# Performance work log

Measured on AMD Instinct MI355X. Metric: run time of the kernel, lower is better.

Reference implementation:

```python
import math
import jax
import jax.numpy as jnp
import numpy as np

GRID = 12  # distance + 1 for distance-11 surface code


def _ln(x, s, b):
    m = jnp.mean(x, axis=-1, keepdims=True)
    v = jnp.mean((x - m) ** 2, axis=-1, keepdims=True)
    return (x - m) / jnp.sqrt(v + 1e-5) * s + b


def _gelu(x):
    return jax.nn.gelu(x, approximate=False)  # torch F.gelu default = exact erf


def _forward(meas, event, leak, event_leak, bias, pm_w, pm_b, pe_w, pe_b, pl_w, pl_b, pel_w, pel_b,
             stab_emb, cyc_emb, er_ln_s, er_ln_b, er_fc1_w, er_fc1_b, er_fc2_w, er_fc2_b,
             ln1_s, ln1_b, Wb, Wq, bq, Wk, bk, Wv, bv, Wo, bo, ln2_s, ln2_b,
             f1_w, f1_b, f2_w, f2_b, conv_w, conv_b, lnf_s, lnf_b,
             P, sc_w, sc_b, dr_w, dr_b, rb1_w, rb1_b, rb2_w, rb2_b, out_w, out_b,
             stab_ids, cycle_ids):
    B, T, S = meas.shape
    L, Hh, _, da = Wq.shape
    dm = Wv.shape[-1]
    d = P.shape[0]

    # per-head additive attention bias, identical across cycles: (L,B,H,S,S)
    Bp = jnp.einsum('bijd,ldh->lbhij', bias, Wb)
    scale = 1.0 / jnp.sqrt(jnp.asarray(da, meas.dtype))
    pos_emb = stab_emb[stab_ids]  # (S, d)

    def embed(t):
        h = (meas[:, t, :, None] * pm_w + pm_b
             + event[:, t, :, None] * pe_w + pe_b
             + leak[:, t, :, None] * pl_w + pl_b
             + event_leak[:, t, :, None] * pel_w + pel_b
             + pos_emb[None] + cyc_emb[cycle_ids[t]][None, None, :])
        for r in range(er_fc1_w.shape[0]):
            hn = _ln(h, er_ln_s[r], er_ln_b[r])
            h = h + jnp.matmul(_gelu(jnp.matmul(hn, er_fc1_w[r]) + er_fc1_b[r]), er_fc2_w[r]) + er_fc2_b[r]
        return h

    X = jnp.zeros((B, S, d), meas.dtype)
    for t in range(T):  # recurrent application of RNNCore over cycles
        X = (X + embed(t)) / jnp.sqrt(jnp.asarray(2.0, meas.dtype))
        for l in range(L):
            Xn = _ln(X, ln1_s[l], ln1_b[l])
            Q = jnp.einsum('bsd,hde->bhse', Xn, Wq[l]) + bq[l][None, :, None, :]
            Kt = jnp.einsum('bsd,hde->bhse', Xn, Wk[l]) + bk[l][None, :, None, :]
            V = jnp.einsum('bsd,hdm->bhsm', Xn, Wv[l]) + bv[l][None, :, None, :]
            Sc = jnp.einsum('bhqe,bhke->bhqk', Q, Kt) + Bp[l]  # bias added BEFORE 1/sqrt(da)
            A = jax.nn.softmax(Sc * scale, axis=-1)
            O = jnp.einsum('bhqk,bhkm->bhqm', A, V)
            Y = O.transpose(0, 2, 1, 3).reshape(B, S, Hh * dm)
            X = X + jnp.matmul(Y, Wo[l]) + bo[l]
            Xn = _ln(X, ln2_s[l], ln2_b[l])
            Yf = jnp.matmul(Xn, f1_w[l]) + f1_b[l]
            a, g = jnp.split(Yf, 2, axis=-1)
            X = X + jnp.matmul(_gelu(a) * g, f2_w[l]) + f2_b[l]
            # conv block: residual depth-mixing Conv1d(k=3, SAME) over the stabilizer axis
            xc = jnp.transpose(X, (0, 2, 1))  # (B, d, S)
            c = jax.lax.conv_general_dilated(xc, conv_w[l], (1,), 'SAME',
                                             dimension_numbers=('NCH', 'OIH', 'NCH'))
            X = X + _gelu(jnp.transpose(c + conv_b[l][None, :, None], (0, 2, 1)))

    # readout
    Xn = _ln(X, lnf_s, lnf_b)
    pad = jnp.broadcast_to(P, (B, GRID * GRID - S, d))  # empty grid cells filled with P
    grid = jnp.concatenate([Xn, pad], axis=1).reshape(B, GRID, GRID, d).transpose(0, 3, 1, 2)
    x = jax.lax.conv_general_dilated(grid, sc_w, (2, 2), 'VALID',
                                     dimension_numbers=('NCHW', 'OIHW', 'NCHW')) + sc_b[None, :, None, None]
    x = _gelu(x)
    x = jnp.einsum('bdhw,rd->brhw', x, dr_w) + dr_b[None, :, None, None]
    x = _gelu(x)
    x = x.mean(axis=2)  # basis 'z': pool over grid rows -> (B, rd, K)
    Kk = x.shape[2]
    x = x.transpose(0, 2, 1).reshape(B * Kk, -1)
    for r in range(rb1_w.shape[0]):
        x = x + jnp.matmul(_gelu(jnp.matmul(x, rb1_w[r]) + rb1_b[r]), rb2_w[r]) + rb2_b[r]
    logits = (jnp.matmul(x, out_w) + out_b).reshape(B, Kk).mean(axis=1)
    return logits


def setup_inputs() -> dict:
    key = jax.random.key(0)
    ks = iter(jax.random.split(key, 100))

    def rn(shape, s=0.02):
        return (s * jax.random.normal(next(ks), shape)).astype(jnp.float32)

    B, T, S, d = 16, 8, 120, 128
    L, H, da, dm, db = 2, 4, 32, 32, 32
    rd, nrb, ncyc = 48, 16, 32
    z = lambda *sh: jnp.zeros(sh, jnp.float32)
    o = lambda *sh: jnp.ones(sh, jnp.float32)
    inp = {
        'meas': jax.random.uniform(next(ks), (B, T, S), jnp.float32),
        'event': jax.random.uniform(next(ks), (B, T, S), jnp.float32),
        'leak': jax.random.uniform(next(ks), (B, T, S), jnp.float32),
        'event_leak': jax.random.uniform(next(ks), (B, T, S), jnp.float32),
        'bias': rn((B, S, S, db), 0.5),
        'pm_w': rn((d,)), 'pm_b': z(d),
        'pe_w': rn((d,)), 'pe_b': z(d),
        'pl_w': rn((d,)), 'pl_b': z(d),
        'pel_w': rn((d,)), 'pel_b': z(d),
        'stab_emb': rn((S, d)),
        'cyc_emb': rn((ncyc, d)),
        'er_ln_s': o(2, d), 'er_ln_b': z(2, d),
        'er_fc1_w': rn((2, d, d)), 'er_fc1_b': z(2, d),
        'er_fc2_w': rn((2, d, d)), 'er_fc2_b': z(2, d),
        'ln1_s': o(L, d), 'ln1_b': z(L, d),
        'Wb': rn((L, db, H)),
        'Wq': rn((L, H, d, da)), 'bq': z(L, H, da),
        'Wk': rn((L, H, d, da)), 'bk': z(L, H, da),
        'Wv': rn((L, H, d, dm)), 'bv': z(L, H, dm),
        'Wo': rn((L, H * dm, d)), 'bo': z(L, d),
        'ln2_s': o(L, d), 'ln2_b': z(L, d),
        'f1_w': rn((L, d, 4 * d)), 'f1_b': z(L, 4 * d),
        'f2_w': rn((L, 2 * d, d)), 'f2_b': z(L, d),
        'conv_w': rn((L, d, d, 3)), 'conv_b': z(L, d),
        'lnf_s': o(d), 'lnf_b': z(d),
        'P': z(d),
        'sc_w': rn((d, d, 2, 2)), 'sc_b': z(d),
        'dr_w': rn((rd, d)), 'dr_b': z(rd),
        'rb1_w': rn((nrb, rd, rd)), 'rb1_b': z(nrb, rd),
        'rb2_w': rn((nrb, rd, rd)), 'rb2_b': z(nrb, rd),
        'out_w': rn((rd,)), 'out_b': z(),
        'stab_ids': jnp.arange(S, dtype=jnp.int32),
        'cycle_ids': jnp.arange(T, dtype=jnp.int32),
    }
    return inp


def reference(meas, event, leak, event_leak, bias, pm_w, pm_b, pe_w, pe_b, pl_w, pl_b, pel_w, pel_b,
              stab_emb, cyc_emb, er_ln_s, er_ln_b, er_fc1_w, er_fc1_b, er_fc2_w, er_fc2_b,
              ln1_s, ln1_b, Wb, Wq, bq, Wk, bk, Wv, bv, Wo, bo, ln2_s, ln2_b,
              f1_w, f1_b, f2_w, f2_b, conv_w, conv_b, lnf_s, lnf_b,
              P, sc_w, sc_b, dr_w, dr_b, rb1_w, rb1_b, rb2_w, rb2_b, out_w, out_b,
              stab_ids, cycle_ids):
    return _forward(meas, event, leak, event_leak, bias, pm_w, pm_b, pe_w, pe_b, pl_w, pl_b, pel_w, pel_b,
                    stab_emb, cyc_emb, er_ln_s, er_ln_b, er_fc1_w, er_fc1_b, er_fc2_w, er_fc2_b,
                    ln1_s, ln1_b, Wb, Wq, bq, Wk, bk, Wv, bv, Wo, bo, ln2_s, ln2_b,
                    f1_w, f1_b, f2_w, f2_b, conv_w, conv_b, lnf_s, lnf_b,
                    P, sc_w, sc_b, dr_w, dr_b, rb1_w, rb1_b, rb2_w, rb2_b, out_w, out_b,
                    stab_ids, cycle_ids)
```

## Files before the change

### kernel.cpp

```cpp
#include <hip/hip_runtime.h>
#include <math.h>

#define Dm 128
#define Ssz 120
#define Bsz 16
#define Tcy 8
#define Hh 4
#define DA 32
#define Lly 2
#define RT 8
#define NRT ((Bsz*Ssz)/RT)
#define NROW (Bsz*Ssz)

struct KParams {
    const float *meas, *event_, *leak, *event_leak, *bias;
    const float *pm_w, *pm_b, *pe_w, *pe_b, *pl_w, *pl_b, *pel_w, *pel_b;
    const float *stab_emb, *cyc_emb;
    const float *er_ln_s, *er_ln_b, *er_fc1_w, *er_fc1_b, *er_fc2_w, *er_fc2_b;
    const float *ln1_s, *ln1_b, *Wb, *Wq, *bq, *Wk, *bk, *Wv, *bv, *Wo, *bo;
    const float *ln2_s, *ln2_b, *f1_w, *f1_b, *f2_w, *f2_b, *conv_w, *conv_b;
    const float *lnf_s, *lnf_b, *Pp, *sc_w, *sc_b, *dr_w, *dr_b;
    const float *rb1_w, *rb1_b, *rb2_w, *rb2_b, *out_w, *out_b;
    const int *stab_ids, *cycle_ids;
    float *Bp, *Q, *K, *V, *G, *Y2, *tmp, *cwT, *E;
};

__device__ __forceinline__ float gelu_f(float x) {
    return 0.5f * x * (1.0f + erff(x * 0.70710678118654752f));
}

__device__ __forceinline__ int swz16(int i, int per_b) {
    return ((((i & 7) << 1) | ((i >> 3) & 1)) * per_b) + (i >> 4);
}

__device__ __forceinline__ void ln_rows8(const float (*src)[Dm], float (*dst)[Dm],
                                         const float* sg, const float* bg, int tid) {
    int r = tid >> 6, g = tid & 63;
    float x0 = src[r][g], x1 = src[r][g + 64];
    float s1 = x0 + x1;
#pragma unroll
    for (int off = 32; off; off >>= 1) s1 += __shfl_xor(s1, off);
    float m = s1 * (1.f / 128.f);
    float d0 = x0 - m, d1 = x1 - m;
    float s2 = d0 * d0 + d1 * d1;
#pragma unroll
    for (int off = 32; off; off >>= 1) s2 += __shfl_xor(s2, off);
    float rstd = rsqrtf(s2 * (1.f / 128.f) + 1e-5f);
    dst[r][g]      = d0 * rstd * sg[g]      + bg[g];
    dst[r][g + 64] = d1 * rstd * sg[g + 64] + bg[g + 64];
}

__device__ __forceinline__ void ln16(const float (*src)[Dm], float (*dst)[Dm],
                                     const float* sg, const float* bg, int tid) {
    int r = tid >> 4, g = tid & 15;
    float v[8];
    float s1 = 0.f;
#pragma unroll
    for (int k = 0; k < 8; k++) { v[k] = src[r][g + 16 * k]; s1 += v[k]; }
#pragma unroll
    for (int off = 8; off; off >>= 1) s1 += __shfl_xor(s1, off);
    float m = s1 * (1.f / 128.f);
    float s2 = 0.f;
#pragma unroll
    for (int k = 0; k < 8; k++) { float d = v[k] - m; s2 += d * d; }
#pragma unroll
    for (int off = 8; off; off >>= 1) s2 += __shfl_xor(s2, off);
    float rstd = rsqrtf(s2 * (1.f / 128.f) + 1e-5f);
#pragma unroll
    for (int k = 0; k < 8; k++)
        dst[r][g + 16 * k] = (v[k] - m) * rstd * sg[g + 16 * k] + bg[g + 16 * k];
}

__global__ __launch_bounds__(256) void k_prepcw(KParams p) {
    int idx = blockIdx.x * 256 + threadIdx.x;
    if (idx >= Lly * Dm * 3 * Dm) return;
    int o = idx & 127; int rest = idx >> 7;
    int k = rest % 3; rest /= 3;
    int i = rest & 127; int l = rest >> 7;
    p.cwT[idx] = p.conv_w[((l * Dm + o) * Dm + i) * 3 + k];
}

__global__ __launch_bounds__(128) void k_bias(KParams p) {
    int blk = blockIdx.x;
    int l = blk / (Bsz * Ssz); int rem = blk % (Bsz * Ssz);
    int b = rem / Ssz, i = rem % Ssz;
    int j = threadIdx.x;
    if (j >= Ssz) return;
    const float4* br4 = (const float4*)(p.bias + ((size_t)(b * Ssz + i) * Ssz + j) * 32);
    float a0 = 0.f, a1 = 0.f, a2 = 0.f, a3 = 0.f;
#pragma unroll
    for (int c4 = 0; c4 < 8; c4++) {
        float bv[4]; *(float4*)bv = br4[c4];
#pragma unroll
        for (int u = 0; u < 4; u++) {
            const float* w = p.Wb + (l * 32 + c4 * 4 + u) * Hh;
            a0 += bv[u] * w[0]; a1 += bv[u] * w[1]; a2 += bv[u] * w[2]; a3 += bv[u] * w[3];
        }
    }
    size_t base = (((size_t)(l * Bsz + b) * Hh) * Ssz + i) * Ssz + j;
    size_t hs = (size_t)Ssz * Ssz;
    p.Bp[base] = a0; p.Bp[base + hs] = a1; p.Bp[base + 2 * hs] = a2; p.Bp[base + 3 * hs] = a3;
}

__global__ __launch_bounds__(256) void k_embed_all(KParams p) {
    __shared__ float h[16][Dm], hn[16][Dm], t1[16][Dm];
    int t = blockIdx.x / 120, tile = blockIdx.x % 120;
    int row0 = tile * 16;
    int tid = threadIdx.x;
    int cid = p.cycle_ids[t];
    for (int idx = tid; idx < 16 * Dm; idx += 256) {
        int r = idx >> 7, j = idx & 127;
        int row = row0 + r;
        int b = row / Ssz, s = row % Ssz;
        int sid = p.stab_ids[s];
        int mi = (b * Tcy + t) * Ssz + s;
        h[r][j] = p.meas[mi] * p.pm_w[j] + p.pm_b[j]
                + p.event_[mi] * p.pe_w[j] + p.pe_b[j]
                + p.leak[mi] * p.pl_w[j] + p.pl_b[j]
                + p.event_leak[mi] * p.pel_w[j] + p.pel_b[j]
                + p.stab_emb[sid * Dm + j] + p.cyc_emb[cid * Dm + j];
    }
    __syncthreads();
    int g2 = tid >> 7, j = tid & 127;
    for (int rbk = 0; rbk < 2; rbk++) {
        ln16(h, hn, p.er_ln_s + rbk * Dm, p.er_ln_b + rbk * Dm, tid);
        __syncthreads();
        const float* W1 = p.er_fc1_w + rbk * Dm * Dm;
        float acc[8];
#pragma unroll
        for (int rr = 0; rr < 8; rr++) acc[rr] = 0.f;
#pragma unroll 2
        for (int i4 = 0; i4 < 32; i4++) {
            float4 xv[8];
#pragma unroll
            for (int rr = 0; rr < 8; rr++) xv[rr] = *(const float4*)&hn[8 * g2 + rr][i4 * 4];
#pragma unroll
            for (int u = 0; u < 4; u++) {
                float w = W1[(i4 * 4 + u) * Dm + j];
#pragma unroll
                for (int rr = 0; rr < 8; rr++) acc[rr] += ((const float*)&xv[rr])[u] * w;
            }
        }
        float b1 = p.er_fc1_b[rbk * Dm + j];
#pragma unroll
        for (int rr = 0; rr < 8; rr++) t1[8 * g2 + rr][j] = gelu_f(acc[rr] + b1);
        __syncthreads();
        const float* W2 = p.er_fc2_w + rbk * Dm * Dm;
#pragma unroll
        for (int rr = 0; rr < 8; rr++) acc[rr] = 0.f;
#pragma unroll 2
        for (int i4 = 0; i4 < 32; i4++) {
            float4 xv[8];
#pragma unroll
            for (int rr = 0; rr < 8; rr++) xv[rr] = *(const float4*)&t1[8 * g2 + rr][i4 * 4];
#pragma unroll
            for (int u = 0; u < 4; u++) {
                float w = W2[(i4 * 4 + u) * Dm + j];
#pragma unroll
                for (int rr = 0; rr < 8; rr++) acc[rr] += ((const float*)&xv[rr])[u] * w;
            }
        }
        float b2 = p.er_fc2_b[rbk * Dm + j];
#pragma unroll
        for (int rr = 0; rr < 8; rr++) h[8 * g2 + rr][j] += acc[rr] + b2;
        __syncthreads();
    }
    for (int idx = tid; idx < 16 * Dm; idx += 256) {
        int r = idx >> 7, jj = idx & 127;
        p.E[((size_t)t * NROW + row0 + r) * Dm + jj] = h[r][jj];
    }
}

__global__ __launch_bounds__(512) void k_qkv(KParams p, float* X, int l, int t, int addE) {
    __shared__ float xn[RT][Dm];
    int rb = swz16(blockIdx.x, Ssz / RT);
    int row0 = rb * RT;
    int b = row0 / Ssz, s0 = row0 % Ssz;
    int tid = threadIdx.x;
    const float inv = 0.70710678118654752f;
    for (int idx = tid; idx < RT * Dm; idx += 512) {
        int r = idx >> 7, j = idx & 127;
        float v = X[(row0 + r) * Dm + j];
        if (addE) {
            v = (v + p.E[((size_t)t * NROW + row0 + r) * Dm + j]) * inv;
            X[(row0 + r) * Dm + j] = v;
        }
        xn[r][j] = v;
    }
    __syncthreads();
    ln_rows8(xn, xn, p.ln1_s + l * Dm, p.ln1_b + l * Dm, tid);
    __syncthreads();
    if (tid < 384) {
        int out = tid >> 7, col = tid & 127;
        int h = col >> 5, e = col & 31;
        const float* W = (out == 0 ? p.Wq : out == 1 ? p.Wk : p.Wv)
                       + ((size_t)(l * Hh + h) * Dm) * DA + e;
        const float* bb = (out == 0 ? p.bq : out == 1 ? p.bk : p.bv) + (l * Hh + h) * DA + e;
        float acc[8];
#pragma unroll
        for (int rr = 0; rr < 8; rr++) acc[rr] = 0.f;
#pragma unroll 2
        for (int i4 = 0; i4 < 32; i4++) {
            float4 xv[8];
#pragma unroll
            for (int rr = 0; rr < 8; rr++) xv[rr] = *(const float4*)&xn[rr][i4 * 4];
#pragma unroll
            for (int u = 0; u < 4; u++) {
                float w = W[(i4 * 4 + u) * DA];
#pragma unroll
                for (int rr = 0; rr < 8; rr++) acc[rr] += ((const float*)&xv[rr])[u] * w;
            }
        }
        float bv = bb[0];
        if (out == 2) {
            float* vb = p.V + ((size_t)(b * Hh + h) * DA + e) * Ssz + s0;
            *(float4*)vb       = make_float4(acc[0] + bv, acc[1] + bv, acc[2] + bv, acc[3] + bv);
            *(float4*)(vb + 4) = make_float4(acc[4] + bv, acc[5] + bv, acc[6] + bv, acc[7] + bv);
        } else {
            float* dst = (out == 0 ? p.Q : p.K);
            size_t base = ((size_t)(b * Hh + h) * Ssz + s0) * DA + e;
#pragma unroll
            for (int rr = 0; rr < 8; rr++) dst[base + rr * DA] = acc[rr] + bv;
        }
    }
}

__global__ __launch_bounds__(512) void k_attn_ffn(KParams p, float* X, int l) {
    __shared__ float4 Kh4[Ssz][8];
    __shared__ float4 Vt4[DA][32];
    __shared__ float sc[RT][Ssz];
    __shared__ float dn[RT];
    __shared__ float Yt[RT][Dm];
    __shared__ float pvp[2][RT][DA];
    __shared__ float opW[2][RT][Dm];
    __shared__ float xres[RT][Dm];
    __shared__ float xn[RT][Dm];
    __shared__ float yfg[RT][256];
    __shared__ float yg[RT][256];
    int rb = swz16(blockIdx.x, Ssz / RT);
    int b = rb / (Ssz / RT), qt = rb % (Ssz / RT);
    int q0 = qt * RT;
    int row0 = rb * RT;
    int tid = threadIdx.x;
    const float scale = 0.17677669529663689f;

    for (int h = 0; h < Hh; h++) {
        __syncthreads();
        {
            const float4* K4 = (const float4*)(p.K + ((size_t)(b * Hh + h) * Ssz) * DA);
            const float4* V4 = (const float4*)(p.V + ((size_t)(b * Hh + h) * DA) * Ssz);
            for (int i = tid; i < 960; i += 512) {
                int k = i >> 3, f = i & 7;
                Kh4[k][f ^ (k & 7)] = K4[i];
                int e = i / 30, s4 = i % 30;
                Vt4[e][s4 ^ (e & 7)] = V4[i];
            }
        }
        __syncthreads();
        {
            int r = tid >> 6, c0 = tid & 63;
            int c1 = c0 + 64;
            bool v1 = c1 < Ssz;
            int sw = c0 & 7;
            const float* Bpr = p.Bp + (((size_t)(l * Bsz + b) * Hh + h) * Ssz + q0 + r) * Ssz;
            const float4* Q4r = (const float4*)(p.Q + ((size_t)(b * Hh + h) * Ssz + q0 + r) * DA);
            float d0 = 0.f, d1 = 0.f;
#pragma unroll
            for (int e4 = 0; e4 < 8; e4++) {
                float4 qv = Q4r[e4];
                float4 k0 = Kh4[c0][e4 ^ sw];
                d0 += qv.x * k0.x + qv.y * k0.y + qv.z * k0.z + qv.w * k0.w;
                if (v1) {
                    float4 k1 = Kh4[c1][e4 ^ sw];
                    d1 += qv.x * k1.x + qv.y * k1.y + qv.z * k1.z + qv.w * k1.w;
                }
            }
            d0 = (d0 + Bpr[c0]) * scale;
            d1 = v1 ? (d1 + Bpr[c1]) * scale : -1e30f;
            float m = fmaxf(d0, d1);
#pragma unroll
            for (int off = 32; off; off >>= 1) m = fmaxf(m, __shfl_xor(m, off));
            float p0 = expf(d0 - m);
            float p1 = v1 ? expf(d1 - m) : 0.f;
            float s = p0 + p1;
#pragma unroll
            for (int off = 32; off; off >>= 1) s += __shfl_xor(s, off);
            sc[r][c0] = p0;
            if (v1) sc[r][c1] = p1;
            if (c0 == 0) dn[r] = s;
        }
        __syncthreads();
        {
            int half = tid >> 8, r = (tid >> 5) & 7, m = tid & 31;
            int sw = m & 7;
            int k40 = half * 15;
            float a = 0.f;
#pragma unroll
            for (int k4 = 0; k4 < 15; k4++) {
                float s4v[4];
                *(float4*)s4v = *(const float4*)&sc[r][(k40 + k4) * 4];
                float4 vv = Vt4[m][(k40 + k4) ^ sw];
                a += s4v[0] * vv.x + s4v[1] * vv.y + s4v[2] * vv.z + s4v[3] * vv.w;
            }
            pvp[half][r][m] = a;
        }
        __syncthreads();
        if (tid < 256) {
            int r = tid >> 5, m = tid & 31;
            Yt[r][h * DA + m] = (pvp[0][r][m] + pvp[1][r][m]) / dn[r];
        }
    }
    __syncthreads();
    int pp = tid >> 8, g = (tid >> 7) & 1, j = tid & 127;
    {
        const float* W = p.Wo + l * Dm * Dm + j;
        float a[4] = {0.f, 0.f, 0.f, 0.f};
        for (int k4 = pp * 16; k4 < pp * 16 + 16; k4++) {
            float4 yv[4];
#pragma unroll
            for (int rr = 0; rr < 4; rr++) yv[rr] = *(const float4*)&Yt[4 * g + rr][k4 * 4];
#pragma unroll
            for (int u = 0; u < 4; u++) {
                float w = W[(k4 * 4 + u) * Dm];
#pragma unroll
                for (int rr = 0; rr < 4; rr++) a[rr] += ((const float*)&yv[rr])[u] * w;
            }
        }
#pragma unroll
        for (int rr = 0; rr < 4; rr++) opW[pp][4 * g + rr][j] = a[rr];
    }
    __syncthreads();
    {
        float bb0 = p.bo[l * Dm + j];
        for (int idx = tid; idx < RT * Dm; idx += 512) {
            int r = idx >> 7, j2 = idx & 127;
            float bb = p.bo[l * Dm + j2];
            float xv = X[(row0 + r) * Dm + j2] + opW[0][r][j2] + opW[1][r][j2] + bb;
            xres[r][j2] = xv;
            xn[r][j2] = xv;
        }
        (void)bb0;
    }
    __syncthreads();
    ln_rows8(xn, xn, p.ln2_s + l * Dm, p.ln2_b + l * Dm, tid);
    __syncthreads();
    {
        const float* W1 = p.f1_w + (size_t)l * Dm * 512 + tid;
        float acc[8];
#pragma unroll
        for (int rr = 0; rr < 8; rr++) acc[rr] = 0.f;
#pragma unroll 2
        for (int i4 = 0; i4 < 32; i4++) {
            float4 xv[8];
#pragma unroll
            for (int rr = 0; rr < 8; rr++) xv[rr] = *(const float4*)&xn[rr][i4 * 4];
#pragma unroll
            for (int u = 0; u < 4; u++) {
                float w = W1[(i4 * 4 + u) * 512];
#pragma unroll
                for (int rr = 0; rr < 8; rr++) acc[rr] += ((const float*)&xv[rr])[u] * w;
            }
        }
        if (tid >= 256) {
#pragma unroll
            for (int rr = 0; rr < 8; rr++) yfg[rr][tid - 256] = acc[rr];
        }
        __syncthreads();
        if (tid < 256) {
            float b1a = p.f1_b[l * 512 + tid];
            float b1g = p.f1_b[l * 512 + 256 + tid];
#pragma unroll
            for (int rr = 0; rr < 8; rr++)
                yg[rr][tid] = gelu_f(acc[rr] + b1a) * (yfg[rr][tid] + b1g);
        }
    }
    __syncthreads();
    {
        const float* W2 = p.f2_w + (size_t)l * 256 * Dm + j;
        float a[4] = {0.f, 0.f, 0.f, 0.f};
        for (int k4 = pp * 32; k4 < pp * 32 + 32; k4++) {
            float4 yv[4];
#pragma unroll
            for (int rr = 0; rr < 4; rr++) yv[rr] = *(const float4*)&yg[4 * g + rr][k4 * 4];
#pragma unroll
            for (int u = 0; u < 4; u++) {
                float w = W2[(k4 * 4 + u) * Dm];
#pragma unroll
                for (int rr = 0; rr < 4; rr++) a[rr] += ((const float*)&yv[rr])[u] * w;
            }
        }
#pragma unroll
        for (int rr = 0; rr < 4; rr++) opW[pp][4 * g + rr][j] = a[rr];
    }
    __syncthreads();
    for (int idx = tid; idx < RT * Dm; idx += 512) {
        int r = idx >> 7, j2 = idx & 127;
        X[(row0 + r) * Dm + j2] = xres[r][j2] + opW[0][r][j2] + opW[1][r][j2] + p.f2_b[l * Dm + j2];
    }
}

__global__ __launch_bounds__(256) void k_conv(KParams p, const float* Xin, float* Xout, int l) {
    __shared__ float xr[RT + 2][Dm];
    int rb = swz16(blockIdx.x, Ssz / RT);
    int row0 = rb * RT;
    int b = row0 / Ssz, s0 = row0 % Ssz;
    int tid = threadIdx.x;
    {
        float4* xr4 = (float4*)&xr[0][0];
        for (int i = tid; i < (RT + 2) * Dm / 4; i += 256) {
            int rr = i >> 5, c = i & 31;
            int s = s0 + rr - 1;
            float4 v = make_float4(0.f, 0.f, 0.f, 0.f);
            if (s >= 0 && s < Ssz) v = *(const float4*)(Xin + (b * Ssz + s) * Dm + 4 * c);
            xr4[i] = v;
        }
    }
    __syncthreads();
    int g = tid >> 7, j = tid & 127;
    const float* CW = p.cwT + (size_t)l * Dm * 3 * Dm + j;
    float a[4] = {0.f, 0.f, 0.f, 0.f};
#pragma unroll 2
    for (int i4 = 0; i4 < 32; i4++) {
        float4 xv[6];
#pragma unroll
        for (int rr = 0; rr < 6; rr++) xv[rr] = *(const float4*)&xr[4 * g + rr][i4 * 4];
#pragma unroll
        for (int u = 0; u < 4; u++) {
            int i = i4 * 4 + u;
            float w0 = CW[(i * 3 + 0) * Dm];
            float w1 = CW[(i * 3 + 1) * Dm];
            float w2 = CW[(i * 3 + 2) * Dm];
#pragma unroll
            for (int rr = 0; rr < 4; rr++)
                a[rr] += w0 * ((const float*)&xv[rr])[u]
                       + w1 * ((const float*)&xv[rr + 1])[u]
                       + w2 * ((const float*)&xv[rr + 2])[u];
        }
    }
    float cb = p.conv_b[l * Dm + j];
#pragma unroll
    for (int rr = 0; rr < 4; rr++)
        Xout[(row0 + 4 * g + rr) * Dm + j] = xr[4 * g + rr + 1][j] + gelu_f(a[rr] + cb);
}

__global__ __launch_bounds__(128) void k_grid(KParams p, const float* X) {
    int blk = swz16(blockIdx.x, 144);
    int b = blk / 144, cell = blk % 144;
    int j = threadIdx.x;
    float* Gr = p.G + (size_t)(b * 144 + cell) * Dm;
    if (cell >= Ssz) { Gr[j] = p.Pp[j]; return; }
    __shared__ float red[4];
    float x = X[(b * Ssz + cell) * Dm + j];
    float s1 = x;
#pragma unroll
    for (int off = 32; off; off >>= 1) s1 += __shfl_xor(s1, off);
    if ((j & 63) == 0) red[j >> 6] = s1;
    __syncthreads();
    float m = (red[0] + red[1]) * (1.f / 128.f);
    float d0 = x - m, s2 = d0 * d0;
#pragma unroll
    for (int off = 32; off; off >>= 1) s2 += __shfl_xor(s2, off);
    if ((j & 63) == 0) red[2 + (j >> 6)] = s2;
    __syncthreads();
    float v = (red[2] + red[3]) * (1.f / 128.f);
    Gr[j] = d0 * rsqrtf(v + 1e-5f) * p.lnf_s[j] + p.lnf_b[j];
}

__global__ __launch_bounds__(128) void k_head(KParams p) {
    int blk = swz16(blockIdx.x, 36);
    int b = blk / 36, r2 = blk % 36, oh = r2 / 6, ow = r2 % 6;
    __shared__ float cells[4][Dm];
    __shared__ float sx[Dm];
    int j = threadIdx.x;
#pragma unroll
    for (int c = 0; c < 4; c++) {
        int kh = c >> 1, kw = c & 1;
        int cell = (2 * oh + kh) * 12 + (2 * ow + kw);
        cells[c][j] = p.G[(size_t)(b * 144 + cell) * Dm + j];
    }
    __syncthreads();
    float acc = p.sc_b[j];
    const float* W = p.sc_w + (size_t)j * Dm * 4;
    for (int i = 0; i < Dm; i++) {
        acc += W[i * 4 + 0] * cells[0][i] + W[i * 4 + 1] * cells[1][i]
             + W[i * 4 + 2] * cells[2][i] + W[i * 4 + 3] * cells[3][i];
    }
    sx[j] = gelu_f(acc);
    __syncthreads();
    if (j < 48) {
        float a = p.dr_b[j];
        const float* w = p.dr_w + j * Dm;
        for (int i = 0; i < Dm; i++) a += sx[i] * w[i];
        p.Y2[((b * 6 + ow) * 6 + oh) * 48 + j] = gelu_f(a);
    }
}

__global__ __launch_bounds__(64) void k_rb(KParams p) {
    int blk = blockIdx.x; int b = blk / 6, ow = blk % 6;
    __shared__ float x[48], t[48];
    int j = threadIdx.x;
    if (j < 48) {
        float s = 0.f;
#pragma unroll
        for (int oh = 0; oh < 6; oh++) s += p.Y2[((b * 6 + ow) * 6 + oh) * 48 + j];
        x[j] = s * (1.f / 6.f);
    }
    __syncthreads();
    for (int r = 0; r < 16; r++) {
        if (j < 48) {
            float a = p.rb1_b[r * 48 + j];
            const float* W = p.rb1_w + (size_t)r * 48 * 48 + j;
            for (int i = 0; i < 48; i++) a += x[i] * W[i * 48];
            t[j] = gelu_f(a);
        }
        __syncthreads();
        if (j < 48) {
            float a = p.rb2_b[r * 48 + j];
            const float* W = p.rb2_w + (size_t)r * 48 * 48 + j;
            for (int i = 0; i < 48; i++) a += t[i] * W[i * 48];
            x[j] += a;
        }
        __syncthreads();
    }
    float pr = (j < 48) ? x[j] * p.out_w[j] : 0.f;
#pragma unroll
    for (int off = 32; off; off >>= 1) pr += __shfl_xor(pr, off);
    if (j == 0) p.tmp[b * 6 + ow] = pr + p.out_b[0];
}

__global__ __launch_bounds__(64) void k_final(KParams p, float* out) {
    int b = threadIdx.x;
    if (b < Bsz) {
        float s = 0.f;
#pragma unroll
        for (int w = 0; w < 6; w++) s += p.tmp[b * 6 + w];
        out[b] = s * (1.f / 6.f);
    }
}

extern "C" void kernel_launch(void* const* d_in, const int* in_sizes, int n_in,
                              void* d_out, int out_size, void* d_ws, size_t ws_size,
                              hipStream_t stream) {
    KParams p;
    p.meas       = (const float*)d_in[0];
    p.event_     = (const float*)d_in[1];
    p.leak       = (const float*)d_in[2];
    p.event_leak = (const float*)d_in[3];
    p.bias       = (const float*)d_in[4];
    p.pm_w  = (const float*)d_in[5];  p.pm_b  = (const float*)d_in[6];
    p.pe_w  = (const float*)d_in[7];  p.pe_b  = (const float*)d_in[8];
    p.pl_w  = (const float*)d_in[9];  p.pl_b  = (const float*)d_in[10];
    p.pel_w = (const float*)d_in[11]; p.pel_b = (const float*)d_in[12];
    p.stab_emb = (const float*)d_in[13];
    p.cyc_emb  = (const float*)d_in[14];
    p.er_ln_s  = (const float*)d_in[15]; p.er_ln_b  = (const float*)d_in[16];
    p.er_fc1_w = (const float*)d_in[17]; p.er_fc1_b = (const float*)d_in[18];
    p.er_fc2_w = (const float*)d_in[19]; p.er_fc2_b = (const float*)d_in[20];
    p.ln1_s = (const float*)d_in[21]; p.ln1_b = (const float*)d_in[22];
    p.Wb = (const float*)d_in[23];
    p.Wq = (const float*)d_in[24]; p.bq = (const float*)d_in[25];
    p.Wk = (const float*)d_in[26]; p.bk = (const float*)d_in[27];
    p.Wv = (const float*)d_in[28]; p.bv = (const float*)d_in[29];
    p.Wo = (const float*)d_in[30]; p.bo = (const float*)d_in[31];
    p.ln2_s = (const float*)d_in[32]; p.ln2_b = (const float*)d_in[33];
    p.f1_w = (const float*)d_in[34]; p.f1_b = (const float*)d_in[35];
    p.f2_w = (const float*)d_in[36]; p.f2_b = (const float*)d_in[37];
    p.conv_w = (const float*)d_in[38]; p.conv_b = (const float*)d_in[39];
    p.lnf_s = (const float*)d_in[40]; p.lnf_b = (const float*)d_in[41];
    p.Pp   = (const float*)d_in[42];
    p.sc_w = (const float*)d_in[43]; p.sc_b = (const float*)d_in[44];
    p.dr_w = (const float*)d_in[45]; p.dr_b = (const float*)d_in[46];
    p.rb1_w = (const float*)d_in[47]; p.rb1_b = (const float*)d_in[48];
    p.rb2_w = (const float*)d_in[49]; p.rb2_b = (const float*)d_in[50];
    p.out_w = (const float*)d_in[51]; p.out_b = (const float*)d_in[52];
    p.stab_ids  = (const int*)d_in[53];
    p.cycle_ids = (const int*)d_in[54];

    float* ws = (float*)d_ws;
    size_t off = 0;
    const size_t BP_SZ  = (size_t)Lly * Bsz * Hh * Ssz * Ssz;
    const size_t QKV_SZ = (size_t)Bsz * Hh * Ssz * DA;
    const size_t X_SZ   = (size_t)Bsz * Ssz * Dm;
    const size_t E_SZ   = (size_t)Tcy * NROW * Dm;
    p.Bp = ws + off; off += BP_SZ;
    p.Q  = ws + off; off += QKV_SZ;
    p.K  = ws + off; off += QKV_SZ;
    p.V  = ws + off; off += QKV_SZ;
    float* X0 = ws + off; off += X_SZ;
    float* X1 = ws + off; off += X_SZ;
    p.G   = ws + off; off += (size_t)Bsz * 144 * Dm;
    p.Y2  = ws + off; off += (size_t)Bsz * 6 * 6 * 48;
    p.tmp = ws + off; off += 96;
    p.cwT = ws + off; off += (size_t)Lly * Dm * 3 * Dm;
    p.E   = ws + off; off += E_SZ;

    hipMemsetAsync(X0, 0, X_SZ * sizeof(float), stream);
    k_prepcw<<<(Lly * Dm * 3 * Dm + 255) / 256, 256, 0, stream>>>(p);
    k_bias<<<Lly * Bsz * Ssz, 128, 0, stream>>>(p);
    k_embed_all<<<Tcy * 120, 256, 0, stream>>>(p);

    float* Xc = X0;
    float* Xa = X1;
    for (int t = 0; t < Tcy; t++) {
        for (int l = 0; l < Lly; l++) {
            k_qkv<<<NRT, 512, 0, stream>>>(p, Xc, l, t, l == 0 ? 1 : 0);
            k_attn_ffn<<<NRT, 512, 0, stream>>>(p, Xc, l);
            k_conv<<<NRT, 256, 0, stream>>>(p, Xc, Xa, l);
            float* tp = Xc; Xc = Xa; Xa = tp;
        }
    }
    k_grid<<<Bsz * 144, 128, 0, stream>>>(p, Xc);
    k_head<<<Bsz * 36, 128, 0, stream>>>(p);
    k_rb<<<Bsz * 6, 64, 0, stream>>>(p);
    k_final<<<1, 64, 0, stream>>>(p, (float*)d_out);
}
```

Baseline: 878.0 us.

## Fuse per-layer QKV, attention/FFN and conv kernels into one persistent kernel

Replaces the 48 separate launches of k_qkv, k_attn_ffn and k_conv across cycles and layers with a single persistent kernel, k_chain, that loops over all steps. Dependencies are handled by per-batch atomic counters and per-block neighbor flags in global memory instead of kernel boundaries. Blocks only wait for blocks of the same batch element, or for their two neighbors before the conv. The conv is folded in with a different work split of 2 rows per thread group. The aim is to remove launch overhead and full-device barriers, at the cost of spin-waiting and a reliance on all 240 blocks being co-resident.

```diff
diff --git a/kernel.cpp b/kernel.cpp
--- a/kernel.cpp
+++ b/kernel.cpp
@@ -11,6 +11,7 @@
 #define RT 8
 #define NRT ((Bsz*Ssz)/RT)
 #define NROW (Bsz*Ssz)
+#define TPB 15
 
 struct KParams {
     const float *meas, *event_, *leak, *event_leak, *bias;
@@ -171,61 +172,7 @@
     }
 }
 
-__global__ __launch_bounds__(512) void k_qkv(KParams p, float* X, int l, int t, int addE) {
-    __shared__ float xn[RT][Dm];
-    int rb = swz16(blockIdx.x, Ssz / RT);
-    int row0 = rb * RT;
-    int b = row0 / Ssz, s0 = row0 % Ssz;
-    int tid = threadIdx.x;
-    const float inv = 0.70710678118654752f;
-    for (int idx = tid; idx < RT * Dm; idx += 512) {
-        int r = idx >> 7, j = idx & 127;
-        float v = X[(row0 + r) * Dm + j];
-        if (addE) {
-            v = (v + p.E[((size_t)t * NROW + row0 + r) * Dm + j]) * inv;
-            X[(row0 + r) * Dm + j] = v;
-        }
-        xn[r][j] = v;
-    }
-    __syncthreads();
-    ln_rows8(xn, xn, p.ln1_s + l * Dm, p.ln1_b + l * Dm, tid);
-    __syncthreads();
-    if (tid < 384) {
-        int out = tid >> 7, col = tid & 127;
-        int h = col >> 5, e = col & 31;
-        const float* W = (out == 0 ? p.Wq : out == 1 ? p.Wk : p.Wv)
-                       + ((size_t)(l * Hh + h) * Dm) * DA + e;
-        const float* bb = (out == 0 ? p.bq : out == 1 ? p.bk : p.bv) + (l * Hh + h) * DA + e;
-        float acc[8];
-#pragma unroll
-        for (int rr = 0; rr < 8; rr++) acc[rr] = 0.f;
-#pragma unroll 2
-        for (int i4 = 0; i4 < 32; i4++) {
-            float4 xv[8];
-#pragma unroll
-            for (int rr = 0; rr < 8; rr++) xv[rr] = *(const float4*)&xn[rr][i4 * 4];
-#pragma unroll
-            for (int u = 0; u < 4; u++) {
-                float w = W[(i4 * 4 + u) * DA];
-#pragma unroll
-                for (int rr = 0; rr < 8; rr++) acc[rr] += ((const float*)&xv[rr])[u] * w;
-            }
-        }
-        float bv = bb[0];
-        if (out == 2) {
-            float* vb = p.V + ((size_t)(b * Hh + h) * DA + e) * Ssz + s0;
-            *(float4*)vb       = make_float4(acc[0] + bv, acc[1] + bv, acc[2] + bv, acc[3] + bv);
-            *(float4*)(vb + 4) = make_float4(acc[4] + bv, acc[5] + bv, acc[6] + bv, acc[7] + bv);
-        } else {
-            float* dst = (out == 0 ? p.Q : p.K);
-            size_t base = ((size_t)(b * Hh + h) * Ssz + s0) * DA + e;
-#pragma unroll
-            for (int rr = 0; rr < 8; rr++) dst[base + rr * DA] = acc[rr] + bv;
-        }
-    }
-}
-
-__global__ __launch_bounds__(512) void k_attn_ffn(KParams p, float* X, int l) {
+__global__ __launch_bounds__(512, 2) void k_chain(KParams p, float* X0, float* X1, int* flags) {
     __shared__ float4 Kh4[Ssz][8];
     __shared__ float4 Vt4[DA][32];
     __shared__ float sc[RT][Ssz];
@@ -237,210 +184,287 @@
     __shared__ float xn[RT][Dm];
     __shared__ float yfg[RT][256];
     __shared__ float yg[RT][256];
-    int rb = swz16(blockIdx.x, Ssz / RT);
-    int b = rb / (Ssz / RT), qt = rb % (Ssz / RT);
+    __shared__ float xr[RT + 2][Dm];
+
+    int rb = swz16(blockIdx.x, TPB);
+    int b = rb / TPB, qt = rb % TPB;
     int q0 = qt * RT;
     int row0 = rb * RT;
     int tid = threadIdx.x;
+    int* flagA = flags;
+    int* flagB = flags + 16;
+    int* blkB  = flags + 32;
     const float scale = 0.17677669529663689f;
-
-    for (int h = 0; h < Hh; h++) {
+    const float inv = 0.70710678118654752f;
+
+    for (int step = 0; step < Tcy * Lly; step++) {
+        int t = step >> 1, l = step & 1;
+        float* Xc = (step & 1) ? X1 : X0;
+        float* Xa = (step & 1) ? X0 : X1;
+
+        if (step > 0) {
+            if (tid == 0) {
+                while (__hip_atomic_load(&flagB[b], __ATOMIC_ACQUIRE, __HIP_MEMORY_SCOPE_AGENT) < TPB * step)
+                    __builtin_amdgcn_s_sleep(2);
+            }
+            __syncthreads();
+        }
+
+        for (int idx = tid; idx < RT * Dm; idx += 512) {
+            int r = idx >> 7, j = idx & 127;
+            float v = Xc[(row0 + r) * Dm + j];
+            if (l == 0) {
+                v = (v + p.E[((size_t)t * NROW + row0 + r) * Dm + j]) * inv;
+                Xc[(row0 + r) * Dm + j] = v;
+            }
+            xn[r][j] = v;
+        }
+        __syncthreads();
+        ln_rows8(xn, xn, p.ln1_s + l * Dm, p.ln1_b + l * Dm, tid);
+        __syncthreads();
+        if (tid < 384) {
+            int out = tid >> 7, col = tid & 127;
+            int h = col >> 5, e = col & 31;
+            const float* W = (out == 0 ? p.Wq : out == 1 ? p.Wk : p.Wv)
+                           + ((size_t)(l * Hh + h) * Dm) * DA + e;
+            const float* bbp = (out == 0 ? p.bq : out == 1 ? p.bk : p.bv) + (l * Hh + h) * DA + e;
+            float acc[8];
+#pragma unroll
+            for (int rr = 0; rr < 8; rr++) acc[rr] = 0.f;
+#pragma unroll 2
+            for (int i4 = 0; i4 < 32; i4++) {
+                float4 xv[8];
+#pragma unroll
+                for (int rr = 0; rr < 8; rr++) xv[rr] = *(const float4*)&xn[rr][i4 * 4];
+#pragma unroll
+                for (int u = 0; u < 4; u++) {
+                    float w = W[(i4 * 4 + u) * DA];
+#pragma unroll
+                    for (int rr = 0; rr < 8; rr++) acc[rr] += ((const float*)&xv[rr])[u] * w;
+                }
+            }
+            float bv = bbp[0];
+            if (out == 2) {
+                float* vb = p.V + ((size_t)(b * Hh + h) * DA + e) * Ssz + q0;
+                *(float4*)vb       = make_float4(acc[0] + bv, acc[1] + bv, acc[2] + bv, acc[3] + bv);
+                *(float4*)(vb + 4) = make_float4(acc[4] + bv, acc[5] + bv, acc[6] + bv, acc[7] + bv);
+            } else {
+                float* dst = (out == 0 ? p.Q : p.K);
+                size_t base = ((size_t)(b * Hh + h) * Ssz + q0) * DA + e;
+#pragma unroll
+                for (int rr = 0; rr < 8; rr++) dst[base + rr * DA] = acc[rr] + bv;
+            }
+        }
+        __syncthreads();
+        if (tid == 0)
+            __hip_atomic_fetch_add(&flagA[b], 1, __ATOMIC_RELEASE, __HIP_MEMORY_SCOPE_AGENT);
+        if (tid == 0) {
+            while (__hip_atomic_load(&flagA[b], __ATOMIC_ACQUIRE, __HIP_MEMORY_SCOPE_AGENT) < TPB * (step + 1))
+                __builtin_amdgcn_s_sleep(2);
+        }
+        __syncthreads();
+
+        for (int h = 0; h < Hh; h++) {
+            __syncthreads();
+            {
+                const float4* K4 = (const float4*)(p.K + ((size_t)(b * Hh + h) * Ssz) * DA);
+                const float4* V4 = (const float4*)(p.V + ((size_t)(b * Hh + h) * DA) * Ssz);
+                for (int i = tid; i < 960; i += 512) {
+                    int k = i >> 3, f = i & 7;
+                    Kh4[k][f ^ (k & 7)] = K4[i];
+                    int e = i / 30, s4 = i % 30;
+                    Vt4[e][s4 ^ (e & 7)] = V4[i];
+                }
+            }
+            __syncthreads();
+            {
+                int r = tid >> 6, c0 = tid & 63;
+                int c1 = c0 + 64;
+                bool v1 = c1 < Ssz;
+                int sw = c0 & 7;
+                const float* Bpr = p.Bp + (((size_t)(l * Bsz + b) * Hh + h) * Ssz + q0 + r) * Ssz;
+                const float4* Q4r = (const float4*)(p.Q + ((size_t)(b * Hh + h) * Ssz + q0 + r) * DA);
+                float d0 = 0.f, d1 = 0.f;
+#pragma unroll
+                for (int e4 = 0; e4 < 8; e4++) {
+                    float4 qv = Q4r[e4];
+                    float4 k0 = Kh4[c0][e4 ^ sw];
+                    d0 += qv.x * k0.x + qv.y * k0.y + qv.z * k0.z + qv.w * k0.w;
+                    if (v1) {
+                        float4 k1 = Kh4[c1][e4 ^ sw];
+                        d1 += qv.x * k1.x + qv.y * k1.y + qv.z * k1.z + qv.w * k1.w;
+                    }
+                }
+                d0 = (d0 + Bpr[c0]) * scale;
+                d1 = v1 ? (d1 + Bpr[c1]) * scale : -1e30f;
+                float m = fmaxf(d0, d1);
+#pragma unroll
+                for (int off = 32; off; off >>= 1) m = fmaxf(m, __shfl_xor(m, off));
+                float p0 = expf(d0 - m);
+                float p1 = v1 ? expf(d1 - m) : 0.f;
+                float s = p0 + p1;
+#pragma unroll
+                for (int off = 32; off; off >>= 1) s += __shfl_xor(s, off);
+                sc[r][c0] = p0;
+                if (v1) sc[r][c1] = p1;
+                if (c0 == 0) dn[r] = s;
+            }
+            __syncthreads();
+            {
+                int half = tid >> 8, r = (tid >> 5) & 7, m = tid & 31;
+                int sw = m & 7;
+                int k40 = half * 15;
+                float a = 0.f;
+#pragma unroll
+                for (int k4 = 0; k4 < 15; k4++) {
+                    float s4v[4];
+                    *(float4*)s4v = *(const float4*)&sc[r][(k40 + k4) * 4];
+                    float4 vv = Vt4[m][(k40 + k4) ^ sw];
+                    a += s4v[0] * vv.x + s4v[1] * vv.y + s4v[2] * vv.z + s4v[3] * vv.w;
+                }
+                pvp[half][r][m] = a;
+            }
+            __syncthreads();
+            if (tid < 256) {
+                int r = tid >> 5, m = tid & 31;
+                Yt[r][h * DA + m] = (pvp[0][r][m] + pvp[1][r][m]) / dn[r];
+            }
+        }
         __syncthreads();
         {
-            const float4* K4 = (const float4*)(p.K + ((size_t)(b * Hh + h) * Ssz) * DA);
-            const float4* V4 = (const float4*)(p.V + ((size_t)(b * Hh + h) * DA) * Ssz);
-            for (int i = tid; i < 960; i += 512) {
-                int k = i >> 3, f = i & 7;
-                Kh4[k][f ^ (k & 7)] = K4[i];
-                int e = i / 30, s4 = i % 30;
-                Vt4[e][s4 ^ (e & 7)] = V4[i];
-            }
-        }
-        __syncthreads();
+            int pp = tid >> 8, g2 = (tid >> 7) & 1, j = tid & 127;
+            {
+                const float* W = p.Wo + l * Dm * Dm + j;
+                float a[4] = {0.f, 0.f, 0.f, 0.f};
+                for (int k4 = pp * 16; k4 < pp * 16 + 16; k4++) {
+                    float4 yv[4];
+#pragma unroll
+                    for (int rr = 0; rr < 4; rr++) yv[rr] = *(const float4*)&Yt[4 * g2 + rr][k4 * 4];
+#pragma unroll
+                    for (int u = 0; u < 4; u++) {
+                        float w = W[(k4 * 4 + u) * Dm];
+#pragma unroll
+                        for (int rr = 0; rr < 4; rr++) a[rr] += ((const float*)&yv[rr])[u] * w;
+                    }
+                }
+#pragma unroll
+                for (int rr = 0; rr < 4; rr++) opW[pp][4 * g2 + rr][j] = a[rr];
+            }
+            __syncthreads();
+            for (int idx = tid; idx < RT * Dm; idx += 512) {
+                int r = idx >> 7, j2 = idx & 127;
+                float xv = Xc[(row0 + r) * Dm + j2] + opW[0][r][j2] + opW[1][r][j2] + p.bo[l * Dm + j2];
+                xres[r][j2] = xv;
+                xn[r][j2] = xv;
+            }
+            __syncthreads();
+            ln_rows8(xn, xn, p.ln2_s + l * Dm, p.ln2_b + l * Dm, tid);
+            __syncthreads();
+            {
+                const float* W1 = p.f1_w + (size_t)l * Dm * 512 + tid;
+                float acc[8];
+#pragma unroll
+                for (int rr = 0; rr < 8; rr++) acc[rr] = 0.f;
+#pragma unroll 2
+                for (int i4 = 0; i4 < 32; i4++) {
+                    float4 xv[8];
+#pragma unroll
+                    for (int rr = 0; rr < 8; rr++) xv[rr] = *(const float4*)&xn[rr][i4 * 4];
+#pragma unroll
+                    for (int u = 0; u < 4; u++) {
+                        float w = W1[(i4 * 4 + u) * 512];
+#pragma unroll
+                        for (int rr = 0; rr < 8; rr++) acc[rr] += ((const float*)&xv[rr])[u] * w;
+                    }
+                }
+                if (tid >= 256) {
+#pragma unroll
+                    for (int rr = 0; rr < 8; rr++) yfg[rr][tid - 256] = acc[rr];
+                }
+                __syncthreads();
+                if (tid < 256) {
+                    float b1a = p.f1_b[l * 512 + tid];
+                    float b1g = p.f1_b[l * 512 + 256 + tid];
+#pragma unroll
+                    for (int rr = 0; rr < 8; rr++)
+                        yg[rr][tid] = gelu_f(acc[rr] + b1a) * (yfg[rr][tid] + b1g);
+                }
+            }
+            __syncthreads();
+            {
+                const float* W2 = p.f2_w + (size_t)l * 256 * Dm + j;
+                float a[4] = {0.f, 0.f, 0.f, 0.f};
+                for (int k4 = pp * 32; k4 < pp * 32 + 32; k4++) {
+                    float4 yv[4];
+#pragma unroll
+                    for (int rr = 0; rr < 4; rr++) yv[rr] = *(const float4*)&yg[4 * g2 + rr][k4 * 4];
+#pragma unroll
+                    for (int u = 0; u < 4; u++) {
+                        float w = W2[(k4 * 4 + u) * Dm];
+#pragma unroll
+                        for (int rr = 0; rr < 4; rr++) a[rr] += ((const float*)&yv[rr])[u] * w;
+                    }
+                }
+#pragma unroll
+                for (int rr = 0; rr < 4; rr++) opW[pp][4 * g2 + rr][j] = a[rr];
+            }
+            __syncthreads();
+            for (int idx = tid; idx < RT * Dm; idx += 512) {
+                int r = idx >> 7, j2 = idx & 127;
+                Xc[(row0 + r) * Dm + j2] = xres[r][j2] + opW[0][r][j2] + opW[1][r][j2] + p.f2_b[l * Dm + j2];
+            }
+        }
+        __syncthreads();
+        if (tid == 0) {
+            __hip_atomic_store(&blkB[rb], step + 1, __ATOMIC_RELEASE, __HIP_MEMORY_SCOPE_AGENT);
+            __hip_atomic_fetch_add(&flagB[b], 1, __ATOMIC_RELEASE, __HIP_MEMORY_SCOPE_AGENT);
+        }
+        if (tid == 0) {
+            if (qt > 0)
+                while (__hip_atomic_load(&blkB[rb - 1], __ATOMIC_ACQUIRE, __HIP_MEMORY_SCOPE_AGENT) < step + 1)
+                    __builtin_amdgcn_s_sleep(2);
+            if (qt < TPB - 1)
+                while (__hip_atomic_load(&blkB[rb + 1], __ATOMIC_ACQUIRE, __HIP_MEMORY_SCOPE_AGENT) < step + 1)
+                    __builtin_amdgcn_s_sleep(2);
+        }
+        __syncthreads();
+
         {
-            int r = tid >> 6, c0 = tid & 63;
-            int c1 = c0 + 64;
-            bool v1 = c1 < Ssz;
-            int sw = c0 & 7;
-            const float* Bpr = p.Bp + (((size_t)(l * Bsz + b) * Hh + h) * Ssz + q0 + r) * Ssz;
-            const float4* Q4r = (const float4*)(p.Q + ((size_t)(b * Hh + h) * Ssz + q0 + r) * DA);
-            float d0 = 0.f, d1 = 0.f;
-#pragma unroll
-            for (int e4 = 0; e4 < 8; e4++) {
-                float4 qv = Q4r[e4];
-                float4 k0 = Kh4[c0][e4 ^ sw];
-                d0 += qv.x * k0.x + qv.y * k0.y + qv.z * k0.z + qv.w * k0.w;
-                if (v1) {
-                    float4 k1 = Kh4[c1][e4 ^ sw];
-                    d1 += qv.x * k1.x + qv.y * k1.y + qv.z * k1.z + qv.w * k1.w;
-                }
-            }
-            d0 = (d0 + Bpr[c0]) * scale;
-            d1 = v1 ? (d1 + Bpr[c1]) * scale : -1e30f;
-            float m = fmaxf(d0, d1);
-#pragma unroll
-            for (int off = 32; off; off >>= 1) m = fmaxf(m, __shfl_xor(m, off));
-            float p0 = expf(d0 - m);
-            float p1 = v1 ? expf(d1 - m) : 0.f;
-            float s = p0 + p1;
-#pragma unroll
-            for (int off = 32; off; off >>= 1) s += __shfl_xor(s, off);
-            sc[r][c0] = p0;
-            if (v1) sc[r][c1] = p1;
-            if (c0 == 0) dn[r] = s;
+            float4* xr4 = (float4*)&xr[0][0];
+            for (int i = tid; i < (RT + 2) * Dm / 4; i += 512) {
+                int rr = i >> 5, c = i & 31;
+                int s = q0 + rr - 1;
+                float4 v = make_float4(0.f, 0.f, 0.f, 0.f);
+                if (s >= 0 && s < Ssz) v = *(const float4*)(Xc + (b * Ssz + s) * Dm + 4 * c);
+                xr4[i] = v;
+            }
         }
         __syncthreads();
         {
-            int half = tid >> 8, r = (tid >> 5) & 7, m = tid & 31;
-            int sw = m & 7;
-            int k40 = half * 15;
-            float a = 0.f;
-#pragma unroll
-            for (int k4 = 0; k4 < 15; k4++) {
-                float s4v[4];
-                *(float4*)s4v = *(const float4*)&sc[r][(k40 + k4) * 4];
-                float4 vv = Vt4[m][(k40 + k4) ^ sw];
-                a += s4v[0] * vv.x + s4v[1] * vv.y + s4v[2] * vv.z + s4v[3] * vv.w;
-            }
-            pvp[half][r][m] = a;
-        }
-        __syncthreads();
-        if (tid < 256) {
-            int r = tid >> 5, m = tid & 31;
-            Yt[r][h * DA + m] = (pvp[0][r][m] + pvp[1][r][m]) / dn[r];
-        }
-    }
-    __syncthreads();
-    int pp = tid >> 8, g = (tid >> 7) & 1, j = tid & 127;
-    {
-        const float* W = p.Wo + l * Dm * Dm + j;
-        float a[4] = {0.f, 0.f, 0.f, 0.f};
-        for (int k4 = pp * 16; k4 < pp * 16 + 16; k4++) {
-            float4 yv[4];
-#pragma unroll
-            for (int rr = 0; rr < 4; rr++) yv[rr] = *(const float4*)&Yt[4 * g + rr][k4 * 4];
-#pragma unroll
-            for (int u = 0; u < 4; u++) {
-                float w = W[(k4 * 4 + u) * Dm];
-#pragma unroll
-                for (int rr = 0; rr < 4; rr++) a[rr] += ((const float*)&yv[rr])[u] * w;
-            }
-        }
-#pragma unroll
-        for (int rr = 0; rr < 4; rr++) opW[pp][4 * g + rr][j] = a[rr];
-    }
-    __syncthreads();
-    {
-        float bb0 = p.bo[l * Dm + j];
-        for (int idx = tid; idx < RT * Dm; idx += 512) {
-            int r = idx >> 7, j2 = idx & 127;
-            float bb = p.bo[l * Dm + j2];
-            float xv = X[(row0 + r) * Dm + j2] + opW[0][r][j2] + opW[1][r][j2] + bb;
-            xres[r][j2] = xv;
-            xn[r][j2] = xv;
-        }
-        (void)bb0;
-    }
-    __syncthreads();
-    ln_rows8(xn, xn, p.ln2_s + l * Dm, p.ln2_b + l * Dm, tid);
-    __syncthreads();
-    {
-        const float* W1 = p.f1_w + (size_t)l * Dm * 512 + tid;
-        float acc[8];
-#pragma unroll
-        for (int rr = 0; rr < 8; rr++) acc[rr] = 0.f;
+            int g2 = tid >> 7, j = tid & 127;
+            const float* CW = p.cwT + (size_t)l * Dm * 3 * Dm + j;
+            float a0 = 0.f, a1 = 0.f;
 #pragma unroll 2
-        for (int i4 = 0; i4 < 32; i4++) {
-            float4 xv[8];
-#pragma unroll
-            for (int rr = 0; rr < 8; rr++) xv[rr] = *(const float4*)&xn[rr][i4 * 4];
-#pragma unroll
-            for (int u = 0; u < 4; u++) {
-                float w = W1[(i4 * 4 + u) * 512];
-#pragma unroll
-                for (int rr = 0; rr < 8; rr++) acc[rr] += ((const float*)&xv[rr])[u] * w;
-            }
-        }
-        if (tid >= 256) {
-#pragma unroll
-            for (int rr = 0; rr < 8; rr++) yfg[rr][tid - 256] = acc[rr];
-        }
-        __syncthreads();
-        if (tid < 256) {
-            float b1a = p.f1_b[l * 512 + tid];
-            float b1g = p.f1_b[l * 512 + 256 + tid];
-#pragma unroll
-            for (int rr = 0; rr < 8; rr++)
-                yg[rr][tid] = gelu_f(acc[rr] + b1a) * (yfg[rr][tid] + b1g);
-        }
-    }
-    __syncthreads();
-    {
-        const float* W2 = p.f2_w + (size_t)l * 256 * Dm + j;
-        float a[4] = {0.f, 0.f, 0.f, 0.f};
-        for (int k4 = pp * 32; k4 < pp * 32 + 32; k4++) {
-            float4 yv[4];
-#pragma unroll
-            for (int rr = 0; rr < 4; rr++) yv[rr] = *(const float4*)&yg[4 * g + rr][k4 * 4];
-#pragma unroll
-            for (int u = 0; u < 4; u++) {
-                float w = W2[(k4 * 4 + u) * Dm];
-#pragma unroll
-                for (int rr = 0; rr < 4; rr++) a[rr] += ((const float*)&yv[rr])[u] * w;
-            }
-        }
-#pragma unroll
-        for (int rr = 0; rr < 4; rr++) opW[pp][4 * g + rr][j] = a[rr];
-    }
-    __syncthreads();
-    for (int idx = tid; idx < RT * Dm; idx += 512) {
-        int r = idx >> 7, j2 = idx & 127;
-        X[(row0 + r) * Dm + j2] = xres[r][j2] + opW[0][r][j2] + opW[1][r][j2] + p.f2_b[l * Dm + j2];
-    }
-}
-
-__global__ __launch_bounds__(256) void k_conv(KParams p, const float* Xin, float* Xout, int l) {
-    __shared__ float xr[RT + 2][Dm];
-    int rb = swz16(blockIdx.x, Ssz / RT);
-    int row0 = rb * RT;
-    int b = row0 / Ssz, s0 = row0 % Ssz;
-    int tid = threadIdx.x;
-    {
-        float4* xr4 = (float4*)&xr[0][0];
-        for (int i = tid; i < (RT + 2) * Dm / 4; i += 256) {
-            int rr = i >> 5, c = i & 31;
-            int s = s0 + rr - 1;
-            float4 v = make_float4(0.f, 0.f, 0.f, 0.f);
-            if (s >= 0 && s < Ssz) v = *(const float4*)(Xin + (b * Ssz + s) * Dm + 4 * c);
-            xr4[i] = v;
-        }
-    }
-    __syncthreads();
-    int g = tid >> 7, j = tid & 127;
-    const float* CW = p.cwT + (size_t)l * Dm * 3 * Dm + j;
-    float a[4] = {0.f, 0.f, 0.f, 0.f};
-#pragma unroll 2
-    for (int i4 = 0; i4 < 32; i4++) {
-        float4 xv[6];
-#pragma unroll
-        for (int rr = 0; rr < 6; rr++) xv[rr] = *(const float4*)&xr[4 * g + rr][i4 * 4];
-#pragma unroll
-        for (int u = 0; u < 4; u++) {
-            int i = i4 * 4 + u;
-            float w0 = CW[(i * 3 + 0) * Dm];
-            float w1 = CW[(i * 3 + 1) * Dm];
-            float w2 = CW[(i * 3 + 2) * Dm];
-#pragma unroll
-            for (int rr = 0; rr < 4; rr++)
-                a[rr] += w0 * ((const float*)&xv[rr])[u]
-                       + w1 * ((const float*)&xv[rr + 1])[u]
-                       + w2 * ((const float*)&xv[rr + 2])[u];
-        }
-    }
-    float cb = p.conv_b[l * Dm + j];
-#pragma unroll
-    for (int rr = 0; rr < 4; rr++)
-        Xout[(row0 + 4 * g + rr) * Dm + j] = xr[4 * g + rr + 1][j] + gelu_f(a[rr] + cb);
+            for (int i4 = 0; i4 < 32; i4++) {
+                float4 xv[4];
+#pragma unroll
+                for (int rr = 0; rr < 4; rr++) xv[rr] = *(const float4*)&xr[2 * g2 + rr][i4 * 4];
+#pragma unroll
+                for (int u = 0; u < 4; u++) {
+                    int i = i4 * 4 + u;
+                    float w0 = CW[(i * 3 + 0) * Dm];
+                    float w1 = CW[(i * 3 + 1) * Dm];
+                    float w2 = CW[(i * 3 + 2) * Dm];
+                    a0 += w0 * ((const float*)&xv[0])[u] + w1 * ((const float*)&xv[1])[u] + w2 * ((const float*)&xv[2])[u];
+                    a1 += w0 * ((const float*)&xv[1])[u] + w1 * ((const float*)&xv[2])[u] + w2 * ((const float*)&xv[3])[u];
+                }
+            }
+            float cb = p.conv_b[l * Dm + j];
+            Xa[(row0 + 2 * g2) * Dm + j]     = xr[2 * g2 + 1][j] + gelu_f(a0 + cb);
+            Xa[(row0 + 2 * g2 + 1) * Dm + j] = xr[2 * g2 + 2][j] + gelu_f(a1 + cb);
+        }
+        __syncthreads();
+    }
 }
 
 __global__ __launch_bounds__(128) void k_grid(KParams p, const float* X) {
@@ -593,23 +617,17 @@
     p.tmp = ws + off; off += 96;
     p.cwT = ws + off; off += (size_t)Lly * Dm * 3 * Dm;
     p.E   = ws + off; off += E_SZ;
+    int* flags = (int*)(ws + off); off += 512;
 
     hipMemsetAsync(X0, 0, X_SZ * sizeof(float), stream);
+    hipMemsetAsync(flags, 0, 512 * sizeof(int), stream);
     k_prepcw<<<(Lly * Dm * 3 * Dm + 255) / 256, 256, 0, stream>>>(p);
     k_bias<<<Lly * Bsz * Ssz, 128, 0, stream>>>(p);
     k_embed_all<<<Tcy * 120, 256, 0, stream>>>(p);
 
-    float* Xc = X0;
-    float* Xa = X1;
-    for (int t = 0; t < Tcy; t++) {
-        for (int l = 0; l < Lly; l++) {
-            k_qkv<<<NRT, 512, 0, stream>>>(p, Xc, l, t, l == 0 ? 1 : 0);
-            k_attn_ffn<<<NRT, 512, 0, stream>>>(p, Xc, l);
-            k_conv<<<NRT, 256, 0, stream>>>(p, Xc, Xa, l);
-            float* tp = Xc; Xc = Xa; Xa = tp;
-        }
-    }
-    k_grid<<<Bsz * 144, 128, 0, stream>>>(p, Xc);
+    k_chain<<<NRT, 512, 0, stream>>>(p, X0, X1, flags);
+
+    k_grid<<<Bsz * 144, 128, 0, stream>>>(p, X0);
     k_head<<<Bsz * 36, 128, 0, stream>>>(p);
     k_rb<<<Bsz * 6, 64, 0, stream>>>(p);
     k_final<<<1, 64, 0, stream>>>(p, (float*)d_out);
```

After: 2.424 ms. 2.76x slower.
